# Kernel optimization log

Hardware: AMD Instinct MI355X
Metric: run time of the kernel (lower is better)

## Reference

```python
import jax, jax.numpy as jnp
import numpy as np

B, T, E, H = 2, 2048, 1024, 16
HD = E // H
EPS = 1e-5


def layer_norm(x, g, b):
    mu = jnp.mean(x, axis=-1, keepdims=True)
    var = jnp.mean(jnp.square(x - mu), axis=-1, keepdims=True)
    return (x - mu) * jax.lax.rsqrt(var + EPS) * g + b


def setup_inputs() -> dict:
    key = jax.random.key(0)
    ks = jax.random.split(key, 12)
    s = 0.02
    return {
        "x": jax.random.normal(ks[0], (B, T, E), jnp.float32),
        "Wk": jax.random.normal(ks[1], (E, E), jnp.float32) * s,
        "Wq": jax.random.normal(ks[2], (E, E), jnp.float32) * s,
        "Wv": jax.random.normal(ks[3], (E, E), jnp.float32) * s,
        "Wp": jax.random.normal(ks[4], (E, E), jnp.float32) * s,
        "bp": jnp.zeros((E,), jnp.float32),
        "W1": jax.random.normal(ks[5], (E, 4 * E), jnp.float32) * s,
        "b1": jnp.zeros((4 * E,), jnp.float32),
        "W2": jax.random.normal(ks[6], (4 * E, E), jnp.float32) * s,
        "b2": jnp.zeros((E,), jnp.float32),
        "g1": jnp.ones((E,), jnp.float32),
        "be1": jnp.zeros((E,), jnp.float32),
        "g2": jnp.ones((E,), jnp.float32),
        "be2": jnp.zeros((E,), jnp.float32),
    }


def reference(x, Wk, Wq, Wv, Wp, bp, W1, b1, W2, b2, g1, be1, g2, be2):
    # --- attention sublayer ---
    h = layer_norm(x, g1, be1)
    q = (h @ Wq).reshape(B, T, H, HD).transpose(0, 2, 1, 3)  # [B,H,T,HD]
    k = (h @ Wk).reshape(B, T, H, HD).transpose(0, 2, 1, 3)
    v = (h @ Wv).reshape(B, T, H, HD).transpose(0, 2, 1, 3)
    scores = jnp.einsum('bhqd,bhkd->bhqk', q, k) * (HD ** -0.5)
    causal = jnp.tril(jnp.ones((T, T), bool))
    scores = jnp.where(causal, scores, -jnp.inf)
    probs = jax.nn.softmax(scores, axis=-1)  # dropout is identity (eval)
    attn = jnp.einsum('bhqk,bhkd->bhqd', probs, v)
    attn = attn.transpose(0, 2, 1, 3).reshape(B, T, E)
    x = x + attn @ Wp + bp
    # --- FFN sublayer ---
    h2 = layer_norm(x, g2, be2)
    ff = jax.nn.relu(h2 @ W1 + b1) @ W2 + b2
    return x + ff
```

## Files before the change

### kernel.cpp

```cpp
#include <hip/hip_runtime.h>
#include <hip/hip_bf16.h>

#define B_ 2
#define T_ 2048
#define E_ 1024
#define H_ 16
#define HD_ 64
#define NT (B_*T_)

typedef __attribute__((ext_vector_type(8))) short s16x8;
typedef __attribute__((ext_vector_type(4))) float f32x4;
typedef __attribute__((ext_vector_type(4))) unsigned int u32x4;

using bf16 = __hip_bfloat16;

#define MFMA16(a,b,c) __builtin_amdgcn_mfma_f32_16x16x32_bf16(a,b,c,0,0,0)

__device__ inline unsigned short f2bf(float f) {
    bf16 h = __float2bfloat16(f);
    return *reinterpret_cast<unsigned short*>(&h);
}

__device__ __forceinline__ unsigned cvt_pk_bf16(float lo, float hi) {
    unsigned r;
    asm("v_cvt_pk_bf16_f32 %0, %1, %2" : "=v"(r) : "v"(lo), "v"(hi));
    return r;
}

__device__ __forceinline__ float exp2_fast(float x) {
    float r;
    asm("v_exp_f32 %0, %1" : "=v"(r) : "v"(x));
    return r;
}

__device__ __forceinline__ void async_cp16(const void* g, void* l) {
    __builtin_amdgcn_global_load_lds((const __attribute__((address_space(1))) void*)g,
                                     (__attribute__((address_space(3))) void*)l,
                                     16, 0, 0);
}

__global__ __launch_bounds__(256) void transpose_all(const float* __restrict__ Wq,
                                                     const float* __restrict__ Wk,
                                                     const float* __restrict__ Wv,
                                                     const float* __restrict__ Wp,
                                                     const float* __restrict__ W1,
                                                     const float* __restrict__ W2,
                                                     bf16* __restrict__ Wqkv_t,
                                                     bf16* __restrict__ W1_t,
                                                     bf16* __restrict__ W2_t) {
    __shared__ float tile[32][33];
    int id = blockIdx.x;
    const float* src; bf16* dst; int K, N, n0, k0;
    float scl = 1.0f;
    if (id < 4096) {
        int z = id >> 10, t = id & 1023;
        src = z == 0 ? Wq : z == 1 ? Wk : z == 2 ? Wv : Wp;
        if (z == 0) scl = 0.125f * 1.44269504088896f;
        dst = Wqkv_t + (size_t)z * 1048576;
        K = 1024; N = 1024; n0 = (t & 31) * 32; k0 = (t >> 5) * 32;
    } else if (id < 8192) {
        int t = id - 4096; src = W1; dst = W1_t; K = 1024; N = 4096;
        n0 = (t & 127) * 32; k0 = (t >> 7) * 32;
    } else {
        int t = id - 8192; src = W2; dst = W2_t; K = 4096; N = 1024;
        n0 = (t & 31) * 32; k0 = (t >> 5) * 32;
    }
    int tx = threadIdx.x, ty = threadIdx.y;
#pragma unroll
    for (int i = 0; i < 4; ++i)
        tile[ty + i*8][tx] = src[(size_t)(k0 + ty + i*8)*N + n0 + tx];
    __syncthreads();
#pragma unroll
    for (int i = 0; i < 4; ++i)
        dst[(size_t)(n0 + ty + i*8)*K + k0 + tx] = __float2bfloat16(tile[tx][ty + i*8] * scl);
}

__global__ __launch_bounds__(256) void ln_kernel(const float* __restrict__ x,
                                                 const float* __restrict__ g,
                                                 const float* __restrict__ b,
                                                 bf16* __restrict__ h) {
    int row = blockIdx.x;
    int tid = threadIdx.x;
    const float4 xv = *reinterpret_cast<const float4*>(x + (size_t)row*E_ + tid*4);
    float s  = xv.x + xv.y + xv.z + xv.w;
    float sq = xv.x*xv.x + xv.y*xv.y + xv.z*xv.z + xv.w*xv.w;
#pragma unroll
    for (int o = 32; o > 0; o >>= 1) { s += __shfl_xor(s, o); sq += __shfl_xor(sq, o); }
    __shared__ float red[8];
    int w = tid >> 6, lane = tid & 63;
    if (lane == 0) { red[w] = s; red[4 + w] = sq; }
    __syncthreads();
    float S = red[0] + red[1] + red[2] + red[3];
    float Q = red[4] + red[5] + red[6] + red[7];
    float mu = S * (1.0f/E_);
    float var = Q * (1.0f/E_) - mu*mu;
    float rs = rsqrtf(var + 1e-5f);
    const float4 gv = *reinterpret_cast<const float4*>(g + tid*4);
    const float4 bv = *reinterpret_cast<const float4*>(b + tid*4);
    ushort4 o4;
    o4.x = f2bf((xv.x - mu)*rs*gv.x + bv.x);
    o4.y = f2bf((xv.y - mu)*rs*gv.y + bv.y);
    o4.z = f2bf((xv.z - mu)*rs*gv.z + bv.z);
    o4.w = f2bf((xv.w - mu)*rs*gv.w + bv.w);
    *reinterpret_cast<ushort4*>(h + (size_t)row*E_ + tid*4) = o4;
}

template<int BM, int BN, int EPI>
__global__ __launch_bounds__(256)
void gemm_t(const bf16* __restrict__ A, const bf16* __restrict__ Bt, void* Cout,
            const float* __restrict__ bias, const float* res,
            int M, int N, int K) {
    constexpr int MT = BM / 32;
    constexpr int NB = BN / 32;
    constexpr int MHALF = BM / 2, NHALF = BN / 2;
    __shared__ bf16 As[BM*64];
    __shared__ bf16 Bs[BN*64];
    int tid = threadIdx.x;
    int lane = tid & 63, w = tid >> 6;
    int wr = w >> 1, wc = w & 1;
    int nbx = gridDim.x;
    int hid = blockIdx.y * nbx + blockIdx.x;
    int cpx = (nbx * gridDim.y) >> 3;
    int nid = (hid & 7) * cpx + (hid >> 3);
    int m0 = (nid / nbx) * BM, n0 = (nid % nbx) * BN;
    int lr = lane & 15, lq = lane >> 4;
    f32x4 acc[MT][NB] = {};
    int srow = w*8 + (lane >> 3);
    int schunk = ((lane & 7) ^ (srow & 7)) * 8;
    const bf16* Ap = A  + (size_t)(m0 + srow)*K + schunk;
    const bf16* Bp = Bt + (size_t)(n0 + srow)*K + schunk;
    for (int k0 = 0; k0 < K; k0 += 64) {
#pragma unroll
        for (int i = 0; i < BM/32; ++i)
            async_cp16(Ap + (size_t)(i*32)*K + k0, (char*)As + i*4096 + w*1024);
#pragma unroll
        for (int i = 0; i < BN/32; ++i)
            async_cp16(Bp + (size_t)(i*32)*K + k0, (char*)Bs + i*4096 + w*1024);
        __syncthreads();
        const char* Asb = (const char*)As;
        const char* Bsb = (const char*)Bs;
        s16x8 af[2][MT], bfr[2][NB];
#pragma unroll
        for (int m = 0; m < MT; ++m) {
            int row = wr*MHALF + m*16 + lr;
            int base = row*128, sw = (row & 7) << 4;
#pragma unroll
            for (int kk = 0; kk < 2; ++kk)
                af[kk][m] = *reinterpret_cast<const s16x8*>(Asb + base + ((kk*64 + lq*16) ^ sw));
        }
#pragma unroll
        for (int n = 0; n < NB; ++n) {
            int row = wc*NHALF + n*16 + lr;
            int base = row*128, sw = (row & 7) << 4;
#pragma unroll
            for (int kk = 0; kk < 2; ++kk)
                bfr[kk][n] = *reinterpret_cast<const s16x8*>(Bsb + base + ((kk*64 + lq*16) ^ sw));
        }
        __builtin_amdgcn_s_setprio(1);
#pragma unroll
        for (int kk = 0; kk < 2; ++kk)
#pragma unroll
            for (int m = 0; m < MT; ++m)
#pragma unroll
                for (int n = 0; n < NB; ++n)
                    acc[m][n] = MFMA16(af[kk][m], bfr[kk][n], acc[m][n]);
        __builtin_amdgcn_s_setprio(0);
        __syncthreads();
    }
#pragma unroll
    for (int m = 0; m < MT; ++m) {
#pragma unroll
        for (int n = 0; n < NB; ++n) {
            int col = n0 + wc*NHALF + n*16 + lr;
#pragma unroll
            for (int r = 0; r < 4; ++r) {
                int row = m0 + wr*MHALF + m*16 + lq*4 + r;
                float v = acc[m][n][r];
                if (EPI == 0) {
                    reinterpret_cast<bf16*>(Cout)[(size_t)row*N + col] = __float2bfloat16(v);
                } else if (EPI == 1) {
                    reinterpret_cast<float*>(Cout)[(size_t)row*N + col] =
                        v + bias[col] + res[(size_t)row*N + col];
                } else {
                    v += bias[col];
                    v = v > 0.f ? v : 0.f;
                    reinterpret_cast<bf16*>(Cout)[(size_t)row*N + col] = __float2bfloat16(v);
                }
            }
        }
    }
}

__global__ __launch_bounds__(256) void v_transpose(const bf16* __restrict__ qkv,
                                                   bf16* __restrict__ Vt) {
    __shared__ unsigned short tile[32][33];
    int tx = threadIdx.x, ty = threadIdx.y;
    int bh = blockIdx.z;
    int b = bh >> 4, h = bh & 15;
    int t0 = blockIdx.x * 32, d0 = blockIdx.y * 32;
    const unsigned short* src = reinterpret_cast<const unsigned short*>(qkv);
#pragma unroll
    for (int i = 0; i < 4; ++i)
        tile[ty + i*8][tx] = src[(size_t)(b*T_ + t0 + ty + i*8)*3072 + 2048 + h*64 + d0 + tx];
    __syncthreads();
    unsigned short* dst = reinterpret_cast<unsigned short*>(Vt);
#pragma unroll
    for (int i = 0; i < 4; ++i)
        dst[(size_t)(bh*64 + d0 + ty + i*8)*T_ + t0 + tx] = tile[tx][ty + i*8];
}

__global__ __launch_bounds__(256)
void flash_attn(const bf16* __restrict__ qkv, const bf16* __restrict__ Vt,
                bf16* __restrict__ O) {
    __shared__ char smem[24576];
    int tid = threadIdx.x;
    int lane = tid & 63, w = tid >> 6;
    int lr = lane & 15, lq = lane >> 4;
    int bh = blockIdx.y, b = bh >> 4, h = bh & 15;
    int pm = (bh & 15) ^ ((bh & 16) ? 31 : 0);
    int qt = (int)(blockIdx.x ^ pm) & 31;
    int q0 = qt * 64;
    int qw = q0 + w * 16;
    const bf16* Qb = qkv + (size_t)(b*T_)*3072 + h*HD_;
    const bf16* Kb = Qb + 1024;
    const bf16* Vb = Vt + (size_t)bh * HD_ * T_;
    char* Pw = smem + 16384 + w*2048;

    int srow_ = w*8 + (lane >> 3);
    int sc_   = (((lane & 7) ^ (srow_ & 7))) * 8;
    const bf16* kS0 = Kb + (size_t)srow_*3072 + sc_;
    const bf16* kS1 = kS0 + (size_t)32*3072;
    const bf16* vS0 = Vb + (size_t)srow_*2048 + sc_;
    const bf16* vS1 = vS0 + (size_t)32*2048;
    char* kD = smem + w*1024;
    char* vD = smem + 8192 + w*1024;

    int sw4 = (lr & 7) << 4;
    int kvo[4], pwo[4];
#pragma unroll
    for (int n = 0; n < 4; ++n) {
        kvo[n] = n*2048 + lr*128 + ((lq << 4) ^ sw4);
        pwo[n] = (lr*128 + n*32 + lq*8) ^ sw4;
    }
    int pao0 = (lr*128 + lq*16) ^ sw4;
    int pao1 = (lr*128 + 64 + lq*16) ^ sw4;

    s16x8 qf[2];
#pragma unroll
    for (int kk = 0; kk < 2; ++kk)
        qf[kk] = *reinterpret_cast<const s16x8*>(Qb + (size_t)(qw + lr)*3072 + kk*32 + lq*8);
    f32x4 od[4] = {};
    const f32x4 Z4 = {0.f, 0.f, 0.f, 0.f};
    float lrun = 0.f;
    int ntiles = qt + 1;

    for (int it = 0; it < ntiles; ++it) {
        async_cp16(kS0, kD);
        async_cp16(kS1, kD + 4096);
        async_cp16(vS0, vD);
        async_cp16(vS1, vD + 4096);
        kS0 += 64*3072; kS1 += 64*3072; vS0 += 64; vS1 += 64;
        __syncthreads();
        const char* Kt = smem;
        const char* Vtl = smem + 8192;
        f32x4 sc[4];
        __builtin_amdgcn_s_setprio(1);
#pragma unroll
        for (int n = 0; n < 4; ++n) {
            s16x8 kf0 = *reinterpret_cast<const s16x8*>(Kt + kvo[n]);
            s16x8 kf1 = *reinterpret_cast<const s16x8*>(Kt + (kvo[n] ^ 64));
            f32x4 z = MFMA16(kf0, qf[0], Z4);
            z = MFMA16(kf1, qf[1], z);
            sc[n] = z;
        }
        __builtin_amdgcn_s_setprio(0);
        if (it == ntiles - 1) {
            int q = qw + lr;
            int kv0 = it * 64;
#pragma unroll
            for (int n = 0; n < 4; ++n)
#pragma unroll
                for (int r = 0; r < 4; ++r)
                    if (kv0 + n*16 + lq*4 + r > q) sc[n][r] = -1e30f;
        }
        float psum = 0.f;
#pragma unroll
        for (int n = 0; n < 4; ++n) {
            float p0 = exp2_fast(sc[n][0]);
            float p1 = exp2_fast(sc[n][1]);
            float p2 = exp2_fast(sc[n][2]);
            float p3 = exp2_fast(sc[n][3]);
            psum += (p0 + p1) + (p2 + p3);
            uint2 pk;
            pk.x = cvt_pk_bf16(p0, p1);
            pk.y = cvt_pk_bf16(p2, p3);
            *reinterpret_cast<uint2*>(Pw + pwo[n]) = pk;
        }
        psum += __shfl_xor(psum, 16);
        psum += __shfl_xor(psum, 32);
        lrun += psum;
        asm volatile("" ::: "memory");
        s16x8 pa0 = *reinterpret_cast<const s16x8*>(Pw + pao0);
        s16x8 pa1 = *reinterpret_cast<const s16x8*>(Pw + pao1);
        __builtin_amdgcn_s_setprio(1);
#pragma unroll
        for (int nd = 0; nd < 4; ++nd) {
            s16x8 vf0 = *reinterpret_cast<const s16x8*>(Vtl + kvo[nd]);
            s16x8 vf1 = *reinterpret_cast<const s16x8*>(Vtl + (kvo[nd] ^ 64));
            od[nd] = MFMA16(pa0, vf0, od[nd]);
            od[nd] = MFMA16(pa1, vf1, od[nd]);
        }
        __builtin_amdgcn_s_setprio(0);
        __syncthreads();
    }
    float lR[4];
#pragma unroll
    for (int r = 0; r < 4; ++r) lR[r] = 1.0f / __shfl(lrun, lq*4 + r);
#pragma unroll
    for (int nd = 0; nd < 4; ++nd) {
#pragma unroll
        for (int r = 0; r < 4; ++r) {
            int row = qw + lq*4 + r;
            O[(size_t)(b*T_ + row)*E_ + h*HD_ + nd*16 + lr] = __float2bfloat16(od[nd][r] * lR[r]);
        }
    }
}

extern "C" void kernel_launch(void* const* d_in, const int* in_sizes, int n_in,
                              void* d_out, int out_size, void* d_ws, size_t ws_size,
                              hipStream_t stream) {
    const float* x   = (const float*)d_in[0];
    const float* Wk  = (const float*)d_in[1];
    const float* Wq  = (const float*)d_in[2];
    const float* Wv  = (const float*)d_in[3];
    const float* Wp  = (const float*)d_in[4];
    const float* bp  = (const float*)d_in[5];
    const float* W1  = (const float*)d_in[6];
    const float* b1  = (const float*)d_in[7];
    const float* W2  = (const float*)d_in[8];
    const float* b2  = (const float*)d_in[9];
    const float* g1  = (const float*)d_in[10];
    const float* be1 = (const float*)d_in[11];
    const float* g2  = (const float*)d_in[12];
    const float* be2 = (const float*)d_in[13];
    float* out = (float*)d_out;

    char* ws = (char*)d_ws;
    bf16* Wqkv_t = (bf16*)(ws + 0);
    bf16* Wp_t   = (bf16*)(ws + 6291456);
    bf16* W1_t   = (bf16*)(ws + 8388608);
    bf16* W2_t   = (bf16*)(ws + 16777216);
    bf16* h      = (bf16*)(ws + 25165824);
    bf16* qkv    = (bf16*)(ws + 33554432);
    bf16* Vt     = (bf16*)(ws + 58720256);
    bf16* attnO  = (bf16*)(ws + 67108864);
    bf16* ff1    = (bf16*)(ws + 33554432);
    float* x2    = (ws_size >= 92274688) ? (float*)(ws + 75497472) : out;

    dim3 tb(32, 8);
    transpose_all<<<12288, tb, 0, stream>>>(Wq, Wk, Wv, Wp, W1, W2, Wqkv_t, W1_t, W2_t);

    ln_kernel<<<NT, 256, 0, stream>>>(x, g1, be1, h);
    gemm_t<128,128,0><<<dim3(24, 32), 256, 0, stream>>>(h, Wqkv_t, qkv, nullptr, nullptr, NT, 3072, 1024);
    v_transpose<<<dim3(64, 2, 32), tb, 0, stream>>>(qkv, Vt);
    flash_attn<<<dim3(32, 32), 256, 0, stream>>>(qkv, Vt, attnO);
    gemm_t<64,64,1><<<dim3(16, 64), 256, 0, stream>>>(attnO, Wp_t, x2, bp, x, NT, 1024, 1024);
    ln_kernel<<<NT, 256, 0, stream>>>(x2, g2, be2, h);
    gemm_t<128,128,2><<<dim3(32, 32), 256, 0, stream>>>(h, W1_t, ff1, b1, nullptr, NT, 4096, 1024);
    gemm_t<64,64,1><<<dim3(16, 64), 256, 0, stream>>>(ff1, W2_t, out, b2, x2, NT, 1024, 4096);
}
```

Before: 204.7 us.

## Replace block-tiled GEMMs with single-wave 64x64 GEMM using triple-buffered async loads

Replaces the 4-wave templated GEMM (128x128 or 64x64 tiles, K-step 64, single-buffered with two barriers per step) with a one-wavefront kernel computing a 64x64 tile. It uses K-step 32 and a three-stage LDS ring fed by async copies, with explicit vmcnt waits instead of __syncthreads. This aims to overlap global loads with MFMA work and remove block-level barriers. In exchange, the large QKV and FFN1 GEMMs lose the 128x128 tile reuse, so global/L2 traffic per FLOP rises and many more small blocks are launched.

```diff
diff --git a/kernel.cpp b/kernel.cpp
--- a/kernel.cpp
+++ b/kernel.cpp
@@ -10,7 +10,6 @@
 
 typedef __attribute__((ext_vector_type(8))) short s16x8;
 typedef __attribute__((ext_vector_type(4))) float f32x4;
-typedef __attribute__((ext_vector_type(4))) unsigned int u32x4;
 
 using bf16 = __hip_bfloat16;
 
@@ -105,76 +104,75 @@
     *reinterpret_cast<ushort4*>(h + (size_t)row*E_ + tid*4) = o4;
 }
 
-template<int BM, int BN, int EPI>
-__global__ __launch_bounds__(256)
-void gemm_t(const bf16* __restrict__ A, const bf16* __restrict__ Bt, void* Cout,
+template<int EPI>
+__global__ __launch_bounds__(64)
+void gemm1w(const bf16* __restrict__ A, const bf16* __restrict__ Bt, void* Cout,
             const float* __restrict__ bias, const float* res,
             int M, int N, int K) {
-    constexpr int MT = BM / 32;
-    constexpr int NB = BN / 32;
-    constexpr int MHALF = BM / 2, NHALF = BN / 2;
-    __shared__ bf16 As[BM*64];
-    __shared__ bf16 Bs[BN*64];
-    int tid = threadIdx.x;
-    int lane = tid & 63, w = tid >> 6;
-    int wr = w >> 1, wc = w & 1;
+    __shared__ bf16 smem[3*4096];
+    int lane = threadIdx.x;
+    int lr = lane & 15, lq = lane >> 4;
     int nbx = gridDim.x;
     int hid = blockIdx.y * nbx + blockIdx.x;
     int cpx = (nbx * gridDim.y) >> 3;
     int nid = (hid & 7) * cpx + (hid >> 3);
-    int m0 = (nid / nbx) * BM, n0 = (nid % nbx) * BN;
-    int lr = lane & 15, lq = lane >> 4;
-    f32x4 acc[MT][NB] = {};
-    int srow = w*8 + (lane >> 3);
-    int schunk = ((lane & 7) ^ (srow & 7)) * 8;
+    int m0 = (nid / nbx) * 64, n0 = (nid % nbx) * 64;
+    f32x4 acc[4][4] = {};
+    int srow = lane >> 2;
+    int schunk = ((lane & 3) ^ (srow & 3)) * 8;
     const bf16* Ap = A  + (size_t)(m0 + srow)*K + schunk;
     const bf16* Bp = Bt + (size_t)(n0 + srow)*K + schunk;
-    for (int k0 = 0; k0 < K; k0 += 64) {
-#pragma unroll
-        for (int i = 0; i < BM/32; ++i)
-            async_cp16(Ap + (size_t)(i*32)*K + k0, (char*)As + i*4096 + w*1024);
-#pragma unroll
-        for (int i = 0; i < BN/32; ++i)
-            async_cp16(Bp + (size_t)(i*32)*K + k0, (char*)Bs + i*4096 + w*1024);
-        __syncthreads();
-        const char* Asb = (const char*)As;
-        const char* Bsb = (const char*)Bs;
-        s16x8 af[2][MT], bfr[2][NB];
-#pragma unroll
-        for (int m = 0; m < MT; ++m) {
-            int row = wr*MHALF + m*16 + lr;
-            int base = row*128, sw = (row & 7) << 4;
-#pragma unroll
-            for (int kk = 0; kk < 2; ++kk)
-                af[kk][m] = *reinterpret_cast<const s16x8*>(Asb + base + ((kk*64 + lq*16) ^ sw));
-        }
-#pragma unroll
-        for (int n = 0; n < NB; ++n) {
-            int row = wc*NHALF + n*16 + lr;
-            int base = row*128, sw = (row & 7) << 4;
-#pragma unroll
-            for (int kk = 0; kk < 2; ++kk)
-                bfr[kk][n] = *reinterpret_cast<const s16x8*>(Bsb + base + ((kk*64 + lq*16) ^ sw));
-        }
-        __builtin_amdgcn_s_setprio(1);
-#pragma unroll
-        for (int kk = 0; kk < 2; ++kk)
-#pragma unroll
-            for (int m = 0; m < MT; ++m)
-#pragma unroll
-                for (int n = 0; n < NB; ++n)
-                    acc[m][n] = MFMA16(af[kk][m], bfr[kk][n], acc[m][n]);
-        __builtin_amdgcn_s_setprio(0);
-        __syncthreads();
-    }
-#pragma unroll
-    for (int m = 0; m < MT; ++m) {
-#pragma unroll
-        for (int n = 0; n < NB; ++n) {
-            int col = n0 + wc*NHALF + n*16 + lr;
+    char* sb = (char*)smem;
+    int nst = K >> 5;
+    int sbuf = 0;
+    auto stage = [&]() {
+#pragma unroll
+        for (int i = 0; i < 4; ++i) {
+            async_cp16(Ap + (size_t)(i*16)*K, sb + sbuf*8192 + i*1024);
+            async_cp16(Bp + (size_t)(i*16)*K, sb + sbuf*8192 + 4096 + i*1024);
+        }
+        Ap += 32; Bp += 32;
+        sbuf = (sbuf == 2) ? 0 : sbuf + 1;
+    };
+    int ka[4];
+#pragma unroll
+    for (int m = 0; m < 4; ++m)
+        ka[m] = (m*16 + lr)*64 + ((lq ^ (lr & 3)) << 4);
+    int cur = 0;
+    auto compute = [&]() {
+        const char* bb = sb + cur*8192;
+        s16x8 af[4], bf[4];
+#pragma unroll
+        for (int m = 0; m < 4; ++m) {
+            af[m] = *reinterpret_cast<const s16x8*>(bb + ka[m]);
+            bf[m] = *reinterpret_cast<const s16x8*>(bb + 4096 + ka[m]);
+        }
+#pragma unroll
+        for (int m = 0; m < 4; ++m)
+#pragma unroll
+            for (int n = 0; n < 4; ++n)
+                acc[m][n] = MFMA16(af[m], bf[n], acc[m][n]);
+        cur = (cur == 2) ? 0 : cur + 1;
+    };
+    stage();
+    stage();
+    for (int t = 0; t < nst - 2; ++t) {
+        stage();
+        asm volatile("s_waitcnt vmcnt(16)" ::: "memory");
+        compute();
+    }
+    asm volatile("s_waitcnt vmcnt(8)" ::: "memory");
+    compute();
+    asm volatile("s_waitcnt vmcnt(0)" ::: "memory");
+    compute();
+#pragma unroll
+    for (int m = 0; m < 4; ++m) {
+#pragma unroll
+        for (int n = 0; n < 4; ++n) {
+            int col = n0 + n*16 + lr;
 #pragma unroll
             for (int r = 0; r < 4; ++r) {
-                int row = m0 + wr*MHALF + m*16 + lq*4 + r;
+                int row = m0 + m*16 + lq*4 + r;
                 float v = acc[m][n][r];
                 if (EPI == 0) {
                     reinterpret_cast<bf16*>(Cout)[(size_t)row*N + col] = __float2bfloat16(v);
@@ -361,11 +359,11 @@
     transpose_all<<<12288, tb, 0, stream>>>(Wq, Wk, Wv, Wp, W1, W2, Wqkv_t, W1_t, W2_t);
 
     ln_kernel<<<NT, 256, 0, stream>>>(x, g1, be1, h);
-    gemm_t<128,128,0><<<dim3(24, 32), 256, 0, stream>>>(h, Wqkv_t, qkv, nullptr, nullptr, NT, 3072, 1024);
+    gemm1w<0><<<dim3(48, 64), 64, 0, stream>>>(h, Wqkv_t, qkv, nullptr, nullptr, NT, 3072, 1024);
     v_transpose<<<dim3(64, 2, 32), tb, 0, stream>>>(qkv, Vt);
     flash_attn<<<dim3(32, 32), 256, 0, stream>>>(qkv, Vt, attnO);
-    gemm_t<64,64,1><<<dim3(16, 64), 256, 0, stream>>>(attnO, Wp_t, x2, bp, x, NT, 1024, 1024);
+    gemm1w<1><<<dim3(16, 64), 64, 0, stream>>>(attnO, Wp_t, x2, bp, x, NT, 1024, 1024);
     ln_kernel<<<NT, 256, 0, stream>>>(x2, g2, be2, h);
-    gemm_t<128,128,2><<<dim3(32, 32), 256, 0, stream>>>(h, W1_t, ff1, b1, nullptr, NT, 4096, 1024);
-    gemm_t<64,64,1><<<dim3(16, 64), 256, 0, stream>>>(ff1, W2_t, out, b2, x2, NT, 1024, 4096);
-}
+    gemm1w<2><<<dim3(64, 64), 64, 0, stream>>>(h, W1_t, ff1, b1, nullptr, NT, 4096, 1024);
+    gemm1w<1><<<dim3(16, 64), 64, 0, stream>>>(ff1, W2_t, out, b2, x2, NT, 1024, 4096);
+}
```

New measurement: 315.3 us. 54.0% more time.

## Add 256x256 eight-wave GEMM kernel for QKV and FFN1 projections

Applied to the files above, without the earlier changes.

Adds a new GEMM kernel with 512 threads and 256x256 output tiles, K-step 32, double-buffered async global-to-LDS copies with a swizzled layout, and s_setprio around the MFMA block. It replaces the 128x128 gemm_t for the QKV and W1 projections to raise data reuse per tile and lower global and LDS traffic per flop. In exchange each block holds 128 accumulator registers per lane, which limits occupancy. The grids also shrink to 192 and 256 blocks, which may leave some of the 256 CUs idle on the QKV launch.

```diff
diff --git a/kernel.cpp b/kernel.cpp
--- a/kernel.cpp
+++ b/kernel.cpp
@@ -10,7 +10,6 @@
 
 typedef __attribute__((ext_vector_type(8))) short s16x8;
 typedef __attribute__((ext_vector_type(4))) float f32x4;
-typedef __attribute__((ext_vector_type(4))) unsigned int u32x4;
 
 using bf16 = __hip_bfloat16;
 
@@ -105,6 +104,103 @@
     *reinterpret_cast<ushort4*>(h + (size_t)row*E_ + tid*4) = o4;
 }
 
+template<int EPI>
+__global__ __launch_bounds__(512)
+void gemm8w(const bf16* __restrict__ A, const bf16* __restrict__ Bt, void* Cout,
+            const float* __restrict__ bias,
+            int M, int N, int K) {
+    __shared__ char smem[65536];
+    int tid = threadIdx.x;
+    int lane = tid & 63, w = tid >> 6;
+    int wm = w >> 2, wn = w & 3;
+    int nbx = gridDim.x;
+    int hid = blockIdx.y * nbx + blockIdx.x;
+    int cpx = (nbx * gridDim.y) >> 3;
+    int nid = (hid & 7) * cpx + (hid >> 3);
+    int m0 = (nid / nbx) * 256, n0 = (nid % nbx) * 256;
+    int lr = lane & 15, lq = lane >> 4;
+    f32x4 acc[8][4] = {};
+    int srow = tid >> 2;
+    int schunk = (((tid & 3) ^ (srow & 3) ^ ((srow >> 2) & 3))) * 8;
+    const bf16* Ap = A  + (size_t)(m0 + srow)*K + schunk;
+    const bf16* Bp = Bt + (size_t)(n0 + srow)*K + schunk;
+    int aoff[8], boff[4];
+#pragma unroll
+    for (int m = 0; m < 8; ++m) {
+        int row = wm*128 + m*16 + lr;
+        aoff[m] = row*64 + (((lq ^ (row & 3) ^ ((row >> 2) & 3))) << 4);
+    }
+#pragma unroll
+    for (int n = 0; n < 4; ++n) {
+        int row = wn*64 + n*16 + lr;
+        boff[n] = 16384 + row*64 + (((lq ^ (row & 3) ^ ((row >> 2) & 3))) << 4);
+    }
+    int nst = K >> 5;
+    auto stage = [&](int buf, int t) {
+        int k0 = t << 5;
+        char* base = smem + buf*32768;
+#pragma unroll
+        for (int i = 0; i < 2; ++i)
+            async_cp16(Ap + (size_t)(i*128)*K + k0, base + i*8192 + w*1024);
+#pragma unroll
+        for (int i = 0; i < 2; ++i)
+            async_cp16(Bp + (size_t)(i*128)*K + k0, base + 16384 + i*8192 + w*1024);
+    };
+    auto compute = [&](int buf) {
+        const char* base = smem + buf*32768;
+        s16x8 af[8], bfr[4];
+#pragma unroll
+        for (int m = 0; m < 8; ++m)
+            af[m] = *reinterpret_cast<const s16x8*>(base + aoff[m]);
+#pragma unroll
+        for (int n = 0; n < 4; ++n)
+            bfr[n] = *reinterpret_cast<const s16x8*>(base + boff[n]);
+        __builtin_amdgcn_s_setprio(1);
+#pragma unroll
+        for (int m = 0; m < 8; ++m)
+#pragma unroll
+            for (int n = 0; n < 4; ++n)
+                acc[m][n] = MFMA16(af[m], bfr[n], acc[m][n]);
+        __builtin_amdgcn_s_setprio(0);
+    };
+    stage(0, 0);
+    for (int t = 0; t < nst; ++t) {
+        int cur = t & 1;
+        if (t + 1 < nst) {
+            stage(cur ^ 1, t + 1);
+            asm volatile("s_waitcnt vmcnt(4)" ::: "memory");
+        } else {
+            asm volatile("s_waitcnt vmcnt(0)" ::: "memory");
+        }
+        __builtin_amdgcn_sched_barrier(0);
+        __builtin_amdgcn_s_barrier();
+        __builtin_amdgcn_sched_barrier(0);
+        compute(cur);
+        __builtin_amdgcn_sched_barrier(0);
+        __builtin_amdgcn_s_barrier();
+        __builtin_amdgcn_sched_barrier(0);
+    }
+#pragma unroll
+    for (int m = 0; m < 8; ++m) {
+#pragma unroll
+        for (int n = 0; n < 4; ++n) {
+            int col = n0 + wn*64 + n*16 + lr;
+#pragma unroll
+            for (int r = 0; r < 4; ++r) {
+                int row = m0 + wm*128 + m*16 + lq*4 + r;
+                float v = acc[m][n][r];
+                if (EPI == 0) {
+                    reinterpret_cast<bf16*>(Cout)[(size_t)row*N + col] = __float2bfloat16(v);
+                } else {
+                    v += bias[col];
+                    v = v > 0.f ? v : 0.f;
+                    reinterpret_cast<bf16*>(Cout)[(size_t)row*N + col] = __float2bfloat16(v);
+                }
+            }
+        }
+    }
+}
+
 template<int BM, int BN, int EPI>
 __global__ __launch_bounds__(256)
 void gemm_t(const bf16* __restrict__ A, const bf16* __restrict__ Bt, void* Cout,
@@ -361,11 +457,11 @@
     transpose_all<<<12288, tb, 0, stream>>>(Wq, Wk, Wv, Wp, W1, W2, Wqkv_t, W1_t, W2_t);
 
     ln_kernel<<<NT, 256, 0, stream>>>(x, g1, be1, h);
-    gemm_t<128,128,0><<<dim3(24, 32), 256, 0, stream>>>(h, Wqkv_t, qkv, nullptr, nullptr, NT, 3072, 1024);
+    gemm8w<0><<<dim3(12, 16), 512, 0, stream>>>(h, Wqkv_t, qkv, nullptr, NT, 3072, 1024);
     v_transpose<<<dim3(64, 2, 32), tb, 0, stream>>>(qkv, Vt);
     flash_attn<<<dim3(32, 32), 256, 0, stream>>>(qkv, Vt, attnO);
     gemm_t<64,64,1><<<dim3(16, 64), 256, 0, stream>>>(attnO, Wp_t, x2, bp, x, NT, 1024, 1024);
     ln_kernel<<<NT, 256, 0, stream>>>(x2, g2, be2, h);
-    gemm_t<128,128,2><<<dim3(32, 32), 256, 0, stream>>>(h, W1_t, ff1, b1, nullptr, NT, 4096, 1024);
+    gemm8w<2><<<dim3(16, 16), 512, 0, stream>>>(h, W1_t, ff1, b1, NT, 4096, 1024);
     gemm_t<64,64,1><<<dim3(16, 64), 256, 0, stream>>>(ff1, W2_t, out, b2, x2, NT, 1024, 4096);
 }
```

Result: slower. 213.6 us (+4.3%).
